# Kernel optimization log

Measured on AMD Instinct MI355X. Metric: run time of the kernel, lower is better.

## Reference

```python
import jax, jax.numpy as jnp
import numpy as np

D = 2048  # input_dimensions (== seq_len, required by the module's math)
H = 8192  # hidden_dimensions
B = 4
S = D


def setup_inputs() -> dict:
    key = jax.random.key(0)
    ks = jax.random.split(key, 13)
    scale_in = 1.0 / np.sqrt(D)
    scale_hid = 1.0 / np.sqrt(H)
    def lin(k, fan_in, fan_out, s):
        return jax.random.normal(k, (fan_in, fan_out), jnp.float32) * s
    inp = {"x": jax.random.normal(ks[0], (B, S, D), jnp.float32)}
    names = ["q", "k", "v"]
    for i, n in enumerate(names):
        inp[f"{n}_w1"] = lin(ks[1 + 4 * i], D, H, scale_in)
        inp[f"{n}_b1"] = jnp.zeros((H,), jnp.float32)
        inp[f"{n}_w2"] = lin(ks[2 + 4 * i], H, D, scale_hid)
        inp[f"{n}_b2"] = jnp.zeros((D,), jnp.float32)
    return inp


def _mlp(x, w1, b1, w2, b2):
    # Linear(D,H) -> ReLU -> Linear(H,D)
    h = jax.nn.relu(jnp.einsum("bsd,dh->bsh", x, w1) + b1)
    return jnp.einsum("bsh,hd->bsd", h, w2) + b2


def reference(x, q_w1, q_b1, q_w2, q_b2, k_w1, k_b1, k_w2, k_b2,
              v_w1, v_b1, v_w2, v_b2):
    Q = _mlp(x, q_w1, q_b1, q_w2, q_b2)
    K = _mlp(x, k_w1, k_b1, k_w2, k_b2)
    V = _mlp(x, v_w1, v_b1, v_w2, v_b2)
    # scores: Q @ K^T  -> [B, S, S]  (no 1/sqrt(d) scaling in original)
    scores = jnp.einsum("bsd,btd->bst", Q, K)
    # nn.Softmax(dim=1): over axis 1 (rows), NOT the usual last axis
    probs = jax.nn.softmax(scores, axis=1)
    # original computes V @ probs (requires S == D)
    out = jnp.einsum("bsd,bdt->bst", V, probs)
    return out
```

## Files before the change

### kernel.cpp

```cpp
#include <hip/hip_runtime.h>
#include <cstdint>
#include <cstddef>

typedef __attribute__((ext_vector_type(8))) short short8;
typedef __attribute__((ext_vector_type(4))) short short4v;
typedef __attribute__((ext_vector_type(4))) float f32x4;
typedef __attribute__((ext_vector_type(4))) int i32x4;

#define DEV __device__ __forceinline__

constexpr int DD = 2048;
constexpr int HHID = 8192;
constexpr int BB = 4;
constexpr int SS = 2048;
constexpr size_t NX = (size_t)BB * SS * DD;
constexpr size_t NW = (size_t)DD * HHID;
constexpr size_t NH = (size_t)BB * SS * HHID;

constexpr size_t OFF_XH = 0;
constexpr size_t OFF_XL = OFF_XH + NX * 2;
constexpr size_t OFF_WH = OFF_XL + NX * 2;
constexpr size_t OFF_WL = OFF_WH + NW * 2;
constexpr size_t OFF_HH = OFF_WL + NW * 2;
constexpr size_t OFF_HL = OFF_HH + NH * 2;
constexpr size_t OFF_QH = OFF_HL + NH * 2;
constexpr size_t OFF_QL = OFF_QH + NX * 2;
constexpr size_t OFF_KH = OFF_QL + NX * 2;
constexpr size_t OFF_KL = OFF_KH + NX * 2;
constexpr size_t OFF_V  = OFF_KL + NX * 2;
constexpr size_t OFF_XS  = OFF_V + NX * 2;
constexpr size_t OFF_WMQ = OFF_XS + 32768;
constexpr size_t OFF_WMK = OFF_WMQ + 32768;
constexpr size_t WS_TOTAL = OFF_WMK + 32768;
constexpr size_t OFF_ST = OFF_HH;
constexpr size_t OFF_PT = OFF_HL;
constexpr size_t OFF_XA1 = OFF_XL;
constexpr size_t OFF_XA2 = OFF_XL + NX;
constexpr size_t OFF_WA1 = OFF_WL;
constexpr size_t OFF_WA2 = OFF_WL + NW;

__device__ __align__(256) unsigned char g_ws[WS_TOTAL];

DEV unsigned char* wsbase(unsigned char* p) { return p ? p : (unsigned char*)g_ws; }
DEV short f2bf(float v) { __bf16 b = (__bf16)v; return __builtin_bit_cast(short, b); }
DEV float bf2f(short s) { return (float)__builtin_bit_cast(__bf16, s); }

DEV void gl16(const short* g, short* l) {
  __builtin_amdgcn_global_load_lds((const __attribute__((address_space(1))) void*)g,
                                   (__attribute__((address_space(3))) void*)l, 16, 0, 0);
}
DEV void gl16b(const signed char* g, signed char* l) {
  __builtin_amdgcn_global_load_lds((const __attribute__((address_space(1))) void*)g,
                                   (__attribute__((address_space(3))) void*)l, 16, 0, 0);
}

__global__ void cast_hi_k(const float* __restrict__ x, unsigned char* wsb,
                          size_t oh, size_t n4) {
  unsigned char* ws = wsbase(wsb);
  short4v* OH = (short4v*)(ws + oh);
  const f32x4* X = (const f32x4*)x;
  for (size_t i = (size_t)blockIdx.x * blockDim.x + threadIdx.x; i < n4;
       i += (size_t)gridDim.x * blockDim.x) {
    const f32x4 v = X[i];
    short4v hs;
#pragma unroll
    for (int e = 0; e < 4; ++e) hs[e] = f2bf(v[e]);
    OH[i] = hs;
  }
}

__launch_bounds__(256)
__global__ void quant_x_k(const float* __restrict__ x, unsigned char* wsb,
// ... 6 lines not shown
  const float* xr = x + (size_t)row * 2048;
  const int tid = threadIdx.x, lane = tid & 63;
  const f32x4 v0 = *(const f32x4*)&xr[tid * 8];
  const f32x4 v1 = *(const f32x4*)&xr[tid * 8 + 4];
  float m = 0.0f;
#pragma unroll
  for (int e = 0; e < 4; ++e) m = fmaxf(m, fmaxf(fabsf(v0[e]), fabsf(v1[e])));
#pragma unroll
  for (int o = 32; o; o >>= 1) m = fmaxf(m, __shfl_xor(m, o));
  __shared__ float rb[4];
  if (lane == 0) rb[tid >> 6] = m;
  __syncthreads();
  m = fmaxf(fmaxf(rb[0], rb[1]), fmaxf(rb[2], rb[3]));
  const float inv = (m > 1e-30f) ? 127.0f / m : 0.0f;
  if (tid == 0) XS[row] = m * (1.0f / 127.0f);
  unsigned int w1a = 0, w1b = 0, w2a = 0, w2b = 0;
#pragma unroll
  for (int e = 0; e < 8; ++e) {
    const float xv = (e < 4) ? v0[e] : v1[e - 4];
    const float q = xv * inv;
    const float a1f = rintf(q);
    int ia2 = (int)rintf((q - a1f) * 256.0f);
    ia2 = ia2 > 127 ? 127 : (ia2 < -127 ? -127 : ia2);
    const unsigned int b1 = (unsigned char)(signed char)(int)a1f;
    const unsigned int b2 = (unsigned char)(signed char)ia2;
    if (e < 4) { w1a |= b1 << (8 * e); w2a |= b2 << (8 * e); }
    else       { w1b |= b1 << (8 * (e - 4)); w2b |= b2 << (8 * (e - 4)); }
  }
  const size_t o = (size_t)row * 2048 + tid * 8;
  *(unsigned int*)&A1[o] = w1a; *(unsigned int*)&A1[o + 4] = w1b;
  *(unsigned int*)&A2[o] = w2a; *(unsigned int*)&A2[o + 4] = w2b;
}

__launch_bounds__(256)
__global__ void colmax_k(const float* __restrict__ w, unsigned char* wsb,
                         size_t omax, int R, int C) {
  unsigned char* ws = wsbase(wsb);
  unsigned int* MX = (unsigned int*)(ws + omax);
  const int col = blockIdx.x * 256 + threadIdx.x;
  const int r0 = blockIdx.y * 128;
  float m = 0.0f;
  for (int r = 0; r < 128; ++r) m = fmaxf(m, fabsf(w[(size_t)(r0 + r) * C + col]));
  atomicMax(&MX[col], __float_as_uint(m));
}

__global__ void transpose_quant_k(const float* __restrict__ src, unsigned char* wsb,
                                  size_t oa1, size_t oa2, size_t omax, int R, int C) {
  __shared__ float t[32][33];
  unsigned char* ws = wsbase(wsb);
  signed char* A1 = (signed char*)(ws + oa1);
  signed char* A2 = (signed char*)(ws + oa2);
  const unsigned int* MX = (const unsigned int*)(ws + omax);
  const int c0 = blockIdx.x << 5, r0 = blockIdx.y << 5;
  const int x = threadIdx.x, y = threadIdx.y;
#pragma unroll
  for (int i = 0; i < 4; ++i) {
    const int rr = y + (i << 3);
    t[rr][x] = src[(size_t)(r0 + rr) * C + c0 + x];
  }
  __syncthreads();
#pragma unroll
  for (int i = 0; i < 4; ++i) {
    const int oc = y + (i << 3);
    const float v = t[x][oc];
    const float mx = __uint_as_float(MX[c0 + oc]);
    const float inv = (mx > 1e-30f) ? 127.0f / mx : 0.0f;
    const float q = v * inv;
    const float a1f = rintf(q);
    int ia2 = (int)rintf((q - a1f) * 256.0f);
    ia2 = ia2 > 127 ? 127 : (ia2 < -127 ? -127 : ia2);
    const size_t o = (size_t)(c0 + oc) * R + r0 + x;
    A1[o] = (signed char)(int)a1f;
    A2[o] = (signed char)ia2;
  }
}

__global__ void transpose_cast_k(const float* __restrict__ src, unsigned char* wsb,
                                 size_t oh, size_t ol, int R, int C, int do_split) {
  __shared__ float t[32][33];
  unsigned char* ws = wsbase(wsb);
  short* OH = (short*)(ws + oh);
  short* OL = (short*)(ws + ol);
  const int c0 = blockIdx.x << 5, r0 = blockIdx.y << 5;
  const int x = threadIdx.x, y = threadIdx.y;
#pragma unroll
  for (int i = 0; i < 4; ++i) {
    const int rr = y + (i << 3);
    t[rr][x] = src[(size_t)(r0 + rr) * C + c0 + x];
  }
  __syncthreads();
#pragma unroll
  for (int i = 0; i < 4; ++i) {
    const int oc = y + (i << 3);
    const float v = t[x][oc];
    const size_t o = (size_t)(c0 + oc) * R + r0 + x;
    const short hb = f2bf(v);
    OH[o] = hb;
    if (do_split) OL[o] = f2bf(v - bf2f(hb));
  }
}

DEV i32x4 mfma_i8(i32x4 a, i32x4 b, i32x4 c) {
  return __builtin_amdgcn_mfma_i32_16x16x64_i8(a, b, c, 0, 0, 0);
}
DEV i32x4 rfi8(const signed char* base, int lstride, int L, int row, int fg) {
  return *(const i32x4*)&base[L * lstride + row * 64 + ((fg ^ ((row >> 1) & 3)) << 4)];
}

__launch_bounds__(512, 2)
__global__ void gemm_i8_k(unsigned char* wsb,
                          size_t xa1o, size_t xa2o, size_t wa1o, size_t wa2o,
                          size_t xso, size_t wmo, const float* __restrict__ bias,
                          size_t ohOff, size_t olOff, int M, int N, int K,
                          int gx, int gxy) {
  __shared__ alignas(16) signed char lds8[114688];

  unsigned char* ws = wsbase(wsb);
  const int tid = threadIdx.x;
  const int lane = tid & 63;
  const int wave = tid >> 6;
  const int wm = (wave >> 2) << 6;
  const int wn = (wave & 3) << 6;
  const int fr = lane & 15;
  const int fg = lane >> 4;

  const int nwg = gridDim.x;
  const int q8 = nwg >> 3;
  const int id = (blockIdx.x & 7) * q8 + (blockIdx.x >> 3);
  const int by = id / gx;
  const int bx = id - by * gx;
  const int brow = by << 7;
  const int bcol = bx << 8;

  const signed char* Xa1 = (const signed char*)(ws + xa1o);
  const signed char* Xa2 = (const signed char*)(ws + xa2o);
  const signed char* Wa1 = (const signed char*)(ws + wa1o);
  const signed char* Wa2 = (const signed char*)(ws + wa2o);
  const float* XS = (const float*)(ws + xso);
  const unsigned int* WM = (const unsigned int*)(ws + wmo);

  const int ar = tid >> 2, ac = tid & 3;
  const size_t aOff = (size_t)(brow + ar) * K + ((ac ^ ((ar >> 1) & 3)) << 4);
  size_t bOff[2];
#pragma unroll
  for (int h = 0; h < 2; ++h) {
    const int G = tid + h * 512;
    const int r = G >> 2, c = G & 3;
    bOff[h] = (size_t)(bcol + r) * K + ((c ^ ((r >> 1) & 3)) << 4);
  }

  auto stageA = [&](int slotBase, int tt) {
    const int ko = tt * 64;
    gl16b(Xa1 + aOff + ko, &lds8[slotBase + (tid << 4)]);
    gl16b(Xa2 + aOff + ko, &lds8[slotBase + 8192 + (tid << 4)]);
  };
  auto stageB = [&](int slotBase, int tt) {
    const int ko = tt * 64;
#pragma unroll
    for (int h = 0; h < 2; ++h) {
      gl16b(Wa1 + bOff[h] + ko, &lds8[slotBase + ((tid + h * 512) << 4)]);
      gl16b(Wa2 + bOff[h] + ko, &lds8[slotBase + 16384 + ((tid + h * 512) << 4)]);
    }
  };

  const int nt = K / 64;
  i32x4 I1[4][4] = {};
  i32x4 I2[4][4] = {};

  stageA(0, 0);
  stageB(49152, 0);
  if (nt > 1) { stageA(16384, 1); stageB(49152 + 32768, 1); }
  if (nt > 1) { asm volatile("s_waitcnt vmcnt(6)" ::: "memory"); }
// ... 23 lines not shown
#pragma unroll
    for (int i = 0; i < 2; ++i)
#pragma unroll
      for (int j = 0; j < 4; ++j) {
        I1[i][j] = mfma_i8(af[i][0], bf[j][0], I1[i][j]);
        I2[i][j] = mfma_i8(af[i][0], bf[j][1], I2[i][j]);
        I2[i][j] = mfma_i8(af[i][1], bf[j][0], I2[i][j]);
      }
    __builtin_amdgcn_s_setprio(0);
    __builtin_amdgcn_s_barrier();

    asm volatile("" ::: "memory");
    if (pf) stageB(sB2, t + 2);
#pragma unroll
    for (int i = 0; i < 2; ++i) {
      af[i][0] = rfi8(aS, 8192, 0, wm + (2 + i) * 16 + fr, fg);
      af[i][1] = rfi8(aS, 8192, 1, wm + (2 + i) * 16 + fr, fg);
    }
    __builtin_amdgcn_s_setprio(1);
#pragma unroll
    for (int i = 0; i < 2; ++i)
#pragma unroll
      for (int j = 0; j < 4; ++j) {
        I1[2 + i][j] = mfma_i8(af[i][0], bf[j][0], I1[2 + i][j]);
        I2[2 + i][j] = mfma_i8(af[i][0], bf[j][1], I2[2 + i][j]);
        I2[2 + i][j] = mfma_i8(af[i][1], bf[j][0], I2[2 + i][j]);
      }
    __builtin_amdgcn_s_setprio(0);
    if (pf) { asm volatile("s_waitcnt vmcnt(6)" ::: "memory"); }
    else    { asm volatile("s_waitcnt vmcnt(0)" ::: "memory"); }
    __builtin_amdgcn_s_barrier();
  }

  short* ldsS = (short*)lds8;
  short* Oh = (short*)(ws + ohOff);
  short* Ol = (short*)(ws + olOff);
  const int fq4 = fg << 2;
#pragma unroll
  for (int rd = 0; rd < 2; ++rd) {
    __builtin_amdgcn_s_barrier();
#pragma unroll
    for (int i = 0; i < 4; ++i) {
      const int rl = wm + i * 16 + fq4;
      const f32x4 xs4 = *(const f32x4*)&XS[brow + rl];
#pragma unroll
      for (int j = 0; j < 4; ++j) {
        const int cl = wn + j * 16 + fr;
        const float wsc = __uint_as_float(WM[bcol + cl]) * (1.0f / 127.0f);
        const float bv = bias[bcol + cl];
#pragma unroll
        for (int e = 0; e < 4; ++e) {
          float u = ((float)I1[i][j][e] + (float)I2[i][j][e] * (1.0f / 256.0f)) *
                        (xs4[e] * wsc) + bv;
          u = fmaxf(u, 0.0f);
          short v;
          if (rd == 0) {
            v = f2bf(u);
          } else {
            const short hb = f2bf(u);
            v = f2bf(u - bf2f(hb));
          }
          ldsS[(rl + e) * 264 + cl] = v;
        }
      }
    }
    __builtin_amdgcn_s_barrier();
    short* gout = (rd == 0) ? Oh : Ol;
#pragma unroll
    for (int gi = 0; gi < 8; ++gi) {
      const int g = gi * 512 + tid;
      const int row = g >> 5, cg = g & 31;
      const short8 v = *(const short8*)&ldsS[row * 264 + cg * 8];
      *(short8*)&gout[(size_t)(brow + row) * N + bcol + cg * 8] = v;
    }
  }
}

constexpr int CH = 8192;

template <int NAB>
DEV short8 read_frag(const short* base, int row, int s, int fg) {
  if constexpr (NAB == 1) {
    return *(const short8*)&base[row * 64 + ((((s << 2) | fg) ^ (row & 7)) << 3)];
  } else {
    return *(const short8*)&base[s * CH + row * 32 + ((fg ^ ((row >> 1) & 3)) << 3)];
  }
}

DEV f32x4 mfma16(short8 a, short8 b, f32x4 c) {
  return __builtin_amdgcn_mfma_f32_16x16x32_bf16(a, b, c, 0, 0, 0);
}

template <int NAB>
DEV void read_half(const short* aBase, int base_row, int fr, int fg, short8 (&av)[4][2]) {
#pragma unroll
  for (int i = 0; i < 4; ++i) {
    const int row = base_row + i * 16 + fr;
    av[i][0] = read_frag<NAB>(aBase, row, 0, fg);
    av[i][1] = read_frag<NAB>(aBase, row, 1, fg);
  }
}

template <int NAB, int H>
DEV void mfma_half(f32x4 (&acc)[8][4], const short8 (&av)[4][2], const short8 (&bfr)[4][2]) {
#pragma unroll
  for (int i = 0; i < 4; ++i)
#pragma unroll
    for (int j = 0; j < 4; ++j) {
      if constexpr (NAB == 1) {
        acc[H * 4 + i][j] = mfma16(av[i][0], bfr[j][0], acc[H * 4 + i][j]);
        acc[H * 4 + i][j] = mfma16(av[i][1], bfr[j][1], acc[H * 4 + i][j]);
      } else {
        acc[H * 4 + i][j] = mfma16(av[i][0], bfr[j][0], acc[H * 4 + i][j]);
        acc[H * 4 + i][j] = mfma16(av[i][0], bfr[j][1], acc[H * 4 + i][j]);
        acc[H * 4 + i][j] = mfma16(av[i][1], bfr[j][0], acc[H * 4 + i][j]);
      }
    }
}

template <int NAB, bool RELU, int STORE>
__launch_bounds__(512, 2)
__global__ void gemm8_k(unsigned char* wsb,
                        size_t aoff0, size_t aoff1, size_t boff0, size_t boff1,
                        const float* __restrict__ bias,
                        size_t ooff0, size_t ooff1, float* __restrict__ optr,
                        int M, int N, int K, int gx, int gxy) {
  constexpr int BK = (NAB == 2) ? 32 : 64;
  __shared__ alignas(16) short lds[10 * CH];

  unsigned char* ws = wsbase(wsb);
  const int tid = threadIdx.x;
  const int lane = tid & 63;
  const int wave = tid >> 6;
  const int wm = (wave >> 2) << 7;
  const int wn = (wave & 3) << 6;

  const int nwg = gridDim.x;
  const int q8 = nwg >> 3;
  const int id = (blockIdx.x & 7) * q8 + (blockIdx.x >> 3);
  const int bz = id / gxy;
  const int rem = id - bz * gxy;
  const int by = rem / gx;
  const int bx = rem - by * gx;
  const int brow = by << 8;
  const int bcol = bx << 8;

  const size_t batchA = (size_t)bz * M * K;
  const size_t batchB = (size_t)bz * N * K;
  const short* A0 = (const short*)(ws + aoff0) + batchA;
  const short* A1 = (const short*)(ws + aoff1) + batchA;
  const short* B0g = (const short*)(ws + boff0) + batchB;
  const short* B1g = (const short*)(ws + boff1) + batchB;

  size_t aSrc[2][2], bSrc[2][2];
#pragma unroll
  for (int h = 0; h < 2; ++h) {
    const int G = tid + h * 512;
    if constexpr (NAB == 1) {
      const int r = G >> 3, c = G & 7;
#pragma unroll
      for (int qq = 0; qq < 2; ++qq) {
        aSrc[qq][h] = (size_t)(brow + qq * 128 + r) * K + (size_t)((c ^ (r & 7)) << 3);
        bSrc[qq][h] = (size_t)(bcol + qq * 128 + r) * K + (size_t)((c ^ (r & 7)) << 3);
      }
    } else {
      const int r = G >> 2, c = G & 3;
      const size_t sw = (size_t)((c ^ ((r >> 1) & 3)) << 3);
      aSrc[0][h] = aSrc[1][h] = (size_t)(brow + r) * K + sw;
      bSrc[0][h] = bSrc[1][h] = (size_t)(bcol + r) * K + sw;
    }
  }
  const int ldst0 = tid << 3;

  auto issueA = [&](int slot, int qq, int tt) {
    short* dst = &lds[slot + qq * CH];
    const short* sp = (NAB == 2) ? (qq ? A1 : A0) : A0;
    const size_t ka = (size_t)tt * BK;
    gl16(sp + aSrc[qq][0] + ka, dst + ldst0);
    gl16(sp + aSrc[qq][1] + ka, dst + ldst0 + CH / 2);
  };
  auto issueB = [&](int slot, int qq, int tt) {
    short* dst = &lds[slot + qq * CH];
    const short* sp = (NAB == 2) ? (qq ? B1g : B0g) : B0g;
    const size_t ka = (size_t)tt * BK;
    gl16(sp + bSrc[qq][0] + ka, dst + ldst0);
    gl16(sp + bSrc[qq][1] + ka, dst + ldst0 + CH / 2);
  };

  const int nt = K / BK;
  const int fr = lane & 15;
  const int fg = lane >> 4;

  f32x4 acc[8][4] = {};

  issueA(0, 0, 0); issueA(0, 1, 0);
  issueB(6 * CH, 0, 0); issueB(6 * CH, 1, 0);
  if (nt > 1) {
    issueA(2 * CH, 0, 1); issueA(2 * CH, 1, 1);
    issueB(8 * CH, 0, 1); issueB(8 * CH, 1, 1);
    asm volatile("s_waitcnt vmcnt(8)" ::: "memory");
  } else {
    asm volatile("s_waitcnt vmcnt(0)" ::: "memory");
  }
  __builtin_amdgcn_s_barrier();

  for (int t = 0; t < nt; ++t) {
    const short* aBase = &lds[(t % 3) * (2 * CH)];
    const short* bBase = &lds[6 * CH + (t & 1) * (2 * CH)];
    const int sA2 = ((t + 2) % 3) * (2 * CH);
    const int sB  = 6 * CH + (t & 1) * (2 * CH);
    const bool pf = (t + 2 < nt);
    short8 bfr[4][2], av[4][2];

    if (pf) { issueA(sA2, 0, t + 2); issueA(sA2, 1, t + 2); }
#pragma unroll
    for (int j = 0; j < 4; ++j) {
      bfr[j][0] = read_frag<NAB>(bBase, wn + j * 16 + fr, 0, fg);
      bfr[j][1] = read_frag<NAB>(bBase, wn + j * 16 + fr, 1, fg);
    }
    read_half<NAB>(aBase, wm, fr, fg, av);
    __builtin_amdgcn_s_setprio(1);
    mfma_half<NAB, 0>(acc, av, bfr);
    __builtin_amdgcn_s_setprio(0);
    __builtin_amdgcn_s_barrier();

    asm volatile("" ::: "memory");
    if (pf) { issueB(sB, 0, t + 2); issueB(sB, 1, t + 2); }
    read_half<NAB>(aBase, wm + 64, fr, fg, av);
    __builtin_amdgcn_s_setprio(1);
    mfma_half<NAB, 1>(acc, av, bfr);
    __builtin_amdgcn_s_setprio(0);
    if (pf) {
      asm volatile("s_waitcnt vmcnt(8)" ::: "memory");
    } else {
      asm volatile("s_waitcnt vmcnt(0)" ::: "memory");
    }
    __builtin_amdgcn_s_barrier();
  }

  const int fq4 = (lane >> 4) << 2;
  if constexpr (STORE == 0 || STORE == 1) {
    short* Oh = (short*)(ws + ooff0);
    short* Ol = (short*)(ws + ooff1);
    constexpr int ROUNDS = (STORE == 0) ? 2 : 1;
#pragma unroll
    for (int rd = 0; rd < ROUNDS; ++rd) {
      __builtin_amdgcn_s_barrier();
#pragma unroll
      for (int i = 0; i < 8; ++i) {
        const int rl = wm + i * 16 + fq4;
#pragma unroll
        for (int j = 0; j < 4; ++j) {
          const int cl = wn + j * 16 + fr;
          const float bv = bias ? bias[bcol + cl] : 0.0f;
#pragma unroll
          for (int e = 0; e < 4; ++e) {
            float u = acc[i][j][e] + bv;
            if constexpr (RELU) u = fmaxf(u, 0.0f);
            short v;
            if (rd == 0) {
              v = f2bf(u);
            } else {
              const short hb = f2bf(u);
              v = f2bf(u - bf2f(hb));
            }
            lds[(rl + e) * 264 + cl] = v;
          }
        }
      }
      __builtin_amdgcn_s_barrier();
      short* gout = (rd == 0) ? Oh : Ol;
#pragma unroll
      for (int gi = 0; gi < 16; ++gi) {
        const int g = gi * 512 + tid;
        const int row = g >> 5, cg = g & 31;
        const short8 v = *(const short8*)&lds[row * 264 + cg * 8];
        *(short8*)&gout[(size_t)(brow + row) * N + bcol + cg * 8] = v;
      }
    }
  } else if constexpr (STORE == 2) {
    float* Of = (float*)(ws + ooff0) + (size_t)bz * M * N;
    float* ldsf = (float*)lds;
#pragma unroll
    for (int h = 0; h < 2; ++h) {
      __builtin_amdgcn_s_barrier();
      if ((wn & 128) == (h << 7)) {
#pragma unroll
        for (int i = 0; i < 8; ++i) {
          const int rl = wm + i * 16 + fq4;
#pragma unroll
          for (int j = 0; j < 4; ++j) {
            const int cp = (wn & 127) + j * 16 + fr;
#pragma unroll
            for (int e = 0; e < 4; ++e)
              ldsf[cp * 258 + rl + e] = acc[i][j][e];
          }
        }
      }
      __builtin_amdgcn_s_barrier();
#pragma unroll
      for (int gi = 0; gi < 16; ++gi) {
        const int g = gi * 512 + tid;
        const int tr = g >> 6, tc4 = (g & 63) << 2;
        const f32x4 v = *(const f32x4*)&ldsf[tr * 258 + tc4];
        *(f32x4*)&Of[(size_t)(bcol + h * 128 + tr) * M + brow + tc4] = v;
      }
    }
  } else {
    float* Op = optr + (size_t)bz * M * N;
    float* ldsf = (float*)lds;
#pragma unroll
    for (int h = 0; h < 2; ++h) {
      __builtin_amdgcn_s_barrier();
      if ((wm & 128) == (h << 7)) {
#pragma unroll
        for (int i = 0; i < 8; ++i) {
          const int rp = (wm & 127) + i * 16 + fq4;
#pragma unroll
          for (int j = 0; j < 4; ++j) {
            const int cl = wn + j * 16 + fr;
#pragma unroll
            for (int e = 0; e < 4; ++e)
              ldsf[(rp + e) * 258 + cl] = acc[i][j][e];
          }
        }
      }
      __builtin_amdgcn_s_barrier();
#pragma unroll
      for (int gi = 0; gi < 16; ++gi) {
        const int g = gi * 512 + tid;
        const int tr = g >> 6, tc4 = (g & 63) << 2;
        const f32x4 v = *(const f32x4*)&ldsf[tr * 258 + tc4];
        *(f32x4*)&Op[(size_t)(brow + h * 128 + tr) * N + bcol + tc4] = v;
      }
    }
  }
}

__launch_bounds__(256)
// ... 28 lines not shown
  short4v o1, o2;
#pragma unroll
  for (int q = 0; q < 4; ++q) { o1[q] = f2bf(e[q] * inv); o2[q] = f2bf(e[4 + q] * inv); }
  out[tid] = o1;
  out[tid + 256] = o2;
}

extern "C" void kernel_launch(void* const* d_in, const int* in_sizes, int n_in,
                              void* d_out, int out_size, void* d_ws, size_t ws_size,
                              hipStream_t stream) {
  const float* x   = (const float*)d_in[0];
  const float* qw1 = (const float*)d_in[1];
  const float* qb1 = (const float*)d_in[2];
  const float* qw2 = (const float*)d_in[3];
  const float* qb2 = (const float*)d_in[4];
  const float* kw1 = (const float*)d_in[5];
  const float* kb1 = (const float*)d_in[6];
  const float* kw2 = (const float*)d_in[7];
  const float* kb2 = (const float*)d_in[8];
  const float* vw1 = (const float*)d_in[9];
  const float* vb1 = (const float*)d_in[10];
  const float* vw2 = (const float*)d_in[11];
  const float* vb2 = (const float*)d_in[12];
  float* out = (float*)d_out;
  unsigned char* wsb = (ws_size >= WS_TOTAL) ? (unsigned char*)d_ws : nullptr;
  unsigned char* wsr;
  if (wsb) wsr = wsb;
  else { hipError_t e = hipGetSymbolAddress((void**)&wsr, HIP_SYMBOL(g_ws)); (void)e; }

  const int M = BB * SS;
  dim3 blk(512);
  dim3 tb(32, 8);

  hipMemsetAsync(wsr + OFF_WMQ, 0, 32768, stream);
  hipMemsetAsync(wsr + OFF_WMK, 0, 32768, stream);

  quant_x_k<<<8192, 256, 0, stream>>>(x, wsb, OFF_XA1, OFF_XA2, OFF_XS);
  cast_hi_k<<<4096, 256, 0, stream>>>(x, wsb, OFF_XH, NX / 4);

  colmax_k<<<dim3(HHID / 256, DD / 128), 256, 0, stream>>>(qw1, wsb, OFF_WMQ, DD, HHID);
  transpose_quant_k<<<dim3(HHID / 32, DD / 32), tb, 0, stream>>>(qw1, wsb, OFF_WA1, OFF_WA2, OFF_WMQ, DD, HHID);
  gemm_i8_k<<<2048, blk, 0, stream>>>(wsb, OFF_XA1, OFF_XA2, OFF_WA1, OFF_WA2,
                                      OFF_XS, OFF_WMQ, qb1, OFF_HH, OFF_HL,
                                      M, HHID, DD, 32, 2048);
  transpose_cast_k<<<dim3(DD / 32, HHID / 32), tb, 0, stream>>>(qw2, wsb, OFF_WH, OFF_WL, HHID, DD, 1);
  gemm8_k<2, false, 0><<<256, blk, 0, stream>>>(
      wsb, OFF_HH, OFF_HL, OFF_WH, OFF_WL, qb2, OFF_QH, OFF_QL, nullptr, M, DD, HHID, 8, 256);

  colmax_k<<<dim3(HHID / 256, DD / 128), 256, 0, stream>>>(kw1, wsb, OFF_WMK, DD, HHID);
  transpose_quant_k<<<dim3(HHID / 32, DD / 32), tb, 0, stream>>>(kw1, wsb, OFF_WA1, OFF_WA2, OFF_WMK, DD, HHID);
  gemm_i8_k<<<2048, blk, 0, stream>>>(wsb, OFF_XA1, OFF_XA2, OFF_WA1, OFF_WA2,
                                      OFF_XS, OFF_WMK, kb1, OFF_HH, OFF_HL,
                                      M, HHID, DD, 32, 2048);
  transpose_cast_k<<<dim3(DD / 32, HHID / 32), tb, 0, stream>>>(kw2, wsb, OFF_WH, OFF_WL, HHID, DD, 1);
  gemm8_k<2, false, 0><<<256, blk, 0, stream>>>(
      wsb, OFF_HH, OFF_HL, OFF_WH, OFF_WL, kb2, OFF_KH, OFF_KL, nullptr, M, DD, HHID, 8, 256);

  transpose_cast_k<<<dim3(HHID / 32, DD / 32), tb, 0, stream>>>(vw1, wsb, OFF_WH, OFF_WL, DD, HHID, 0);
  gemm8_k<1, true, 1><<<1024, blk, 0, stream>>>(
      wsb, OFF_XH, 0, OFF_WH, 0, vb1, OFF_HH, 0, nullptr, M, HHID, DD, 32, 1024);
  transpose_cast_k<<<dim3(DD / 32, HHID / 32), tb, 0, stream>>>(vw2, wsb, OFF_WH, OFF_WL, HHID, DD, 0);
  gemm8_k<1, false, 1><<<256, blk, 0, stream>>>(
      wsb, OFF_HH, 0, OFF_WH, 0, vb2, OFF_V, 0, nullptr, M, DD, HHID, 8, 256);

  gemm8_k<2, false, 2><<<256, blk, 0, stream>>>(
      wsb, OFF_QH, OFF_QL, OFF_KH, OFF_KL, nullptr, OFF_ST, 0, nullptr, SS, SS, DD, 8, 64);

  softmax_rows_k<<<BB * SS, 256, 0, stream>>>(wsb, OFF_ST, OFF_PT);

  gemm8_k<1, false, 3><<<256, blk, 0, stream>>>(
      wsb, OFF_V, 0, OFF_PT, 0, nullptr, 0, 0, out, SS, SS, DD, 8, 64);
}
```

Before: 3.066 ms.

## Move Q/K second-layer and score GEMMs from split-bf16 to split-int8 MFMA

Moves the Q and K second-layer GEMMs and the QK^T score GEMM off the three-pass split-bf16 path and onto the split-int8 (a1 + a2/256) MFMA kernel. To feed it, the change adds per-row quantization kernels for the hidden activations and for Q/K, per-column weight quantization for w2, a scale-fix pass, and a batched transposed fp32 store variant in gemm_i8_k. The aim is to replace three bf16 MFMAs per tile with two int8 MFMAs at higher throughput. In exchange it adds extra quantization passes over the large H buffer and changes numerical precision.

```diff
diff --git a/kernel.cpp b/kernel.cpp
--- a/kernel.cpp
+++ b/kernel.cpp
@@ -17,27 +17,31 @@
 constexpr size_t NW = (size_t)DD * HHID;
 constexpr size_t NH = (size_t)BB * SS * HHID;
 
-constexpr size_t OFF_XH = 0;
-constexpr size_t OFF_XL = OFF_XH + NX * 2;
-constexpr size_t OFF_WH = OFF_XL + NX * 2;
-constexpr size_t OFF_WL = OFF_WH + NW * 2;
-constexpr size_t OFF_HH = OFF_WL + NW * 2;
-constexpr size_t OFF_HL = OFF_HH + NH * 2;
-constexpr size_t OFF_QH = OFF_HL + NH * 2;
-constexpr size_t OFF_QL = OFF_QH + NX * 2;
-constexpr size_t OFF_KH = OFF_QL + NX * 2;
-constexpr size_t OFF_KL = OFF_KH + NX * 2;
-constexpr size_t OFF_V  = OFF_KL + NX * 2;
+constexpr size_t OFF_XH  = 0;
+constexpr size_t OFF_XA1 = OFF_XH + NX * 2;
+constexpr size_t OFF_XA2 = OFF_XA1 + NX;
+constexpr size_t OFF_WA1 = OFF_XA2 + NX;
+constexpr size_t OFF_WA2 = OFF_WA1 + NW;
+constexpr size_t OFF_WHV = OFF_WA1;
+constexpr size_t OFF_HH  = OFF_WA2 + NW;
+constexpr size_t OFF_HL  = OFF_HH + NH * 2;
+constexpr size_t OFF_QKH = OFF_HL + NH * 2;
+constexpr size_t OFF_QKL = OFF_QKH + NX * 2;
+constexpr size_t OFF_QA1 = OFF_QKL + NX * 2;
+constexpr size_t OFF_QA2 = OFF_QA1 + NX;
+constexpr size_t OFF_KA1 = OFF_QA2 + NX;
+constexpr size_t OFF_KA2 = OFF_KA1 + NX;
+constexpr size_t OFF_HA1 = OFF_KA2 + NX;
+constexpr size_t OFF_HA2 = OFF_HA1 + NH;
+constexpr size_t OFF_V   = OFF_HA2 + NH;
 constexpr size_t OFF_XS  = OFF_V + NX * 2;
-constexpr size_t OFF_WMQ = OFF_XS + 32768;
-constexpr size_t OFF_WMK = OFF_WMQ + 32768;
-constexpr size_t WS_TOTAL = OFF_WMK + 32768;
+constexpr size_t OFF_HS  = OFF_XS + 32768;
+constexpr size_t OFF_QS  = OFF_HS + 32768;
+constexpr size_t OFF_KS  = OFF_QS + 32768;
+constexpr size_t OFF_CM  = OFF_KS + 32768;
+constexpr size_t WS_TOTAL = OFF_CM + 32768;
 constexpr size_t OFF_ST = OFF_HH;
 constexpr size_t OFF_PT = OFF_HL;
-constexpr size_t OFF_XA1 = OFF_XL;
-constexpr size_t OFF_XA2 = OFF_XL + NX;
-constexpr size_t OFF_WA1 = OFF_WL;
-constexpr size_t OFF_WA2 = OFF_WL + NW;
 
 __device__ __align__(256) unsigned char g_ws[WS_TOTAL];
 
@@ -110,6 +114,48 @@
   *(unsigned int*)&A2[o] = w2a; *(unsigned int*)&A2[o + 4] = w2b;
 }
 
+__launch_bounds__(1024)
+__global__ void rowquant_k(unsigned char* wsb, size_t hho, size_t hlo,
+                           size_t oa1, size_t oa2, size_t oso, int rowlen) {
+  unsigned char* ws = wsbase(wsb);
+  const int row = blockIdx.x, tid = threadIdx.x, lane = tid & 63, wv = tid >> 6;
+  const int nw = blockDim.x >> 6;
+  const short8 hi = *((const short8*)((const short*)(ws + hho) + (size_t)row * rowlen) + tid);
+  const short8 lo = *((const short8*)((const short*)(ws + hlo) + (size_t)row * rowlen) + tid);
+  float v[8]; float m = 0.0f;
+#pragma unroll
+  for (int e = 0; e < 8; ++e) {
+    v[e] = bf2f(hi[e]) + bf2f(lo[e]);
+    m = fmaxf(m, fabsf(v[e]));
+  }
+#pragma unroll
+  for (int o = 32; o; o >>= 1) m = fmaxf(m, __shfl_xor(m, o));
+  __shared__ float rb[16];
+  if (lane == 0) rb[wv] = m;
+  __syncthreads();
+  m = rb[0];
+  for (int i = 1; i < nw; ++i) m = fmaxf(m, rb[i]);
+  const float inv = (m > 1e-30f) ? 127.0f / m : 0.0f;
+  if (tid == 0) ((float*)(ws + oso))[row] = m * (1.0f / 127.0f);
+  unsigned int w1a = 0, w1b = 0, w2a = 0, w2b = 0;
+#pragma unroll
+  for (int e = 0; e < 8; ++e) {
+    const float q = v[e] * inv;
+    const float a1f = rintf(q);
+    int ia2 = (int)rintf((q - a1f) * 256.0f);
+    ia2 = ia2 > 127 ? 127 : (ia2 < -127 ? -127 : ia2);
+    const unsigned int b1 = (unsigned char)(signed char)(int)a1f;
+    const unsigned int b2 = (unsigned char)(signed char)ia2;
+    if (e < 4) { w1a |= b1 << (8 * e); w2a |= b2 << (8 * e); }
+    else       { w1b |= b1 << (8 * (e - 4)); w2b |= b2 << (8 * (e - 4)); }
+  }
+  const size_t o = (size_t)row * rowlen + tid * 8;
+  signed char* A1 = (signed char*)(ws + oa1);
+  signed char* A2 = (signed char*)(ws + oa2);
+  *(unsigned int*)&A1[o] = w1a; *(unsigned int*)&A1[o + 4] = w1b;
+  *(unsigned int*)&A2[o] = w2a; *(unsigned int*)&A2[o + 4] = w2b;
+}
+
 __launch_bounds__(256)
 __global__ void colmax_k(const float* __restrict__ w, unsigned char* wsb,
                          size_t omax, int R, int C) {
@@ -122,13 +168,23 @@
   atomicMax(&MX[col], __float_as_uint(m));
 }
 
+__global__ void scalefix_k(unsigned char* wsb, size_t off, int n) {
+  unsigned char* ws = wsbase(wsb);
+  const int i = blockIdx.x * 256 + threadIdx.x;
+  if (i < n) {
+    float* p = (float*)(ws + off);
+    const unsigned int u = ((const unsigned int*)p)[i];
+    p[i] = __uint_as_float(u) * (1.0f / 127.0f);
+  }
+}
+
 __global__ void transpose_quant_k(const float* __restrict__ src, unsigned char* wsb,
-                                  size_t oa1, size_t oa2, size_t omax, int R, int C) {
+                                  size_t oa1, size_t oa2, size_t osc, int R, int C) {
   __shared__ float t[32][33];
   unsigned char* ws = wsbase(wsb);
   signed char* A1 = (signed char*)(ws + oa1);
   signed char* A2 = (signed char*)(ws + oa2);
-  const unsigned int* MX = (const unsigned int*)(ws + omax);
+  const float* SC = (const float*)(ws + osc);
   const int c0 = blockIdx.x << 5, r0 = blockIdx.y << 5;
   const int x = threadIdx.x, y = threadIdx.y;
 #pragma unroll
@@ -141,8 +197,8 @@
   for (int i = 0; i < 4; ++i) {
     const int oc = y + (i << 3);
     const float v = t[x][oc];
-    const float mx = __uint_as_float(MX[c0 + oc]);
-    const float inv = (mx > 1e-30f) ? 127.0f / mx : 0.0f;
+    const float s = SC[c0 + oc];
+    const float inv = (s > 1e-38f) ? 1.0f / s : 0.0f;
     const float q = v * inv;
     const float a1f = rintf(q);
     int ia2 = (int)rintf((q - a1f) * 256.0f);
@@ -154,11 +210,10 @@
 }
 
 __global__ void transpose_cast_k(const float* __restrict__ src, unsigned char* wsb,
-                                 size_t oh, size_t ol, int R, int C, int do_split) {
+                                 size_t oh, int R, int C) {
   __shared__ float t[32][33];
   unsigned char* ws = wsbase(wsb);
   short* OH = (short*)(ws + oh);
-  short* OL = (short*)(ws + ol);
   const int c0 = blockIdx.x << 5, r0 = blockIdx.y << 5;
   const int x = threadIdx.x, y = threadIdx.y;
 #pragma unroll
@@ -170,11 +225,7 @@
 #pragma unroll
   for (int i = 0; i < 4; ++i) {
     const int oc = y + (i << 3);
-    const float v = t[x][oc];
-    const size_t o = (size_t)(c0 + oc) * R + r0 + x;
-    const short hb = f2bf(v);
-    OH[o] = hb;
-    if (do_split) OL[o] = f2bf(v - bf2f(hb));
+    OH[(size_t)(c0 + oc) * R + r0 + x] = f2bf(t[x][oc]);
   }
 }
 
@@ -185,11 +236,12 @@
   return *(const i32x4*)&base[L * lstride + row * 64 + ((fg ^ ((row >> 1) & 3)) << 4)];
 }
 
+template <bool RELU, int STORE>
 __launch_bounds__(512, 2)
 __global__ void gemm_i8_k(unsigned char* wsb,
-                          size_t xa1o, size_t xa2o, size_t wa1o, size_t wa2o,
-                          size_t xso, size_t wmo, const float* __restrict__ bias,
-                          size_t ohOff, size_t olOff, int M, int N, int K,
+                          size_t a1o, size_t a2o, size_t b1o, size_t b2o,
+                          size_t aso, size_t bso, const float* __restrict__ bias,
+                          size_t o0, size_t o1, int M, int N, int K,
                           int gx, int gxy) {
   __shared__ alignas(16) signed char lds8[114688];
 
@@ -205,17 +257,21 @@
   const int nwg = gridDim.x;
   const int q8 = nwg >> 3;
   const int id = (blockIdx.x & 7) * q8 + (blockIdx.x >> 3);
-  const int by = id / gx;
-  const int bx = id - by * gx;
+  const int bz = id / gxy;
+  const int rem = id - bz * gxy;
+  const int by = rem / gx;
+  const int bx = rem - by * gx;
   const int brow = by << 7;
   const int bcol = bx << 8;
 
-  const signed char* Xa1 = (const signed char*)(ws + xa1o);
-  const signed char* Xa2 = (const signed char*)(ws + xa2o);
-  const signed char* Wa1 = (const signed char*)(ws + wa1o);
-  const signed char* Wa2 = (const signed char*)(ws + wa2o);
-  const float* XS = (const float*)(ws + xso);
-  const unsigned int* WM = (const unsigned int*)(ws + wmo);
+  const size_t batchA = (size_t)bz * M * K;
+  const size_t batchB = (STORE == 2) ? (size_t)bz * N * K : 0;
+  const signed char* Xa1 = (const signed char*)(ws + a1o) + batchA;
+  const signed char* Xa2 = (const signed char*)(ws + a2o) + batchA;
+  const signed char* Wa1 = (const signed char*)(ws + b1o) + batchB;
+  const signed char* Wa2 = (const signed char*)(ws + b2o) + batchB;
+  const float* AS = (const float*)(ws + aso) + (size_t)bz * M;
+  const float* BS = (const float*)(ws + bso) + ((STORE == 2) ? (size_t)bz * N : 0);
 
   const int ar = tid >> 2, ac = tid & 3;
   const size_t aOff = (size_t)(brow + ar) * K + ((ac ^ ((ar >> 1) & 3)) << 4);
@@ -305,100 +361,102 @@
     __builtin_amdgcn_s_barrier();
   }
 
-  short* ldsS = (short*)lds8;
-  short* Oh = (short*)(ws + ohOff);
-  short* Ol = (short*)(ws + olOff);
   const int fq4 = fg << 2;
-#pragma unroll
-  for (int rd = 0; rd < 2; ++rd) {
-    __builtin_amdgcn_s_barrier();
-#pragma unroll
-    for (int i = 0; i < 4; ++i) {
-      const int rl = wm + i * 16 + fq4;
-      const f32x4 xs4 = *(const f32x4*)&XS[brow + rl];
-#pragma unroll
-      for (int j = 0; j < 4; ++j) {
-        const int cl = wn + j * 16 + fr;
-        const float wsc = __uint_as_float(WM[bcol + cl]) * (1.0f / 127.0f);
-        const float bv = bias[bcol + cl];
-#pragma unroll
-        for (int e = 0; e < 4; ++e) {
-          float u = ((float)I1[i][j][e] + (float)I2[i][j][e] * (1.0f / 256.0f)) *
-                        (xs4[e] * wsc) + bv;
-          u = fmaxf(u, 0.0f);
-          short v;
-          if (rd == 0) {
-            v = f2bf(u);
-          } else {
-            const short hb = f2bf(u);
-            v = f2bf(u - bf2f(hb));
+  if constexpr (STORE == 0) {
+    short* ldsS = (short*)lds8;
+    short* Oh = (short*)(ws + o0);
+    short* Ol = (short*)(ws + o1);
+#pragma unroll
+    for (int rd = 0; rd < 2; ++rd) {
+      __builtin_amdgcn_s_barrier();
+#pragma unroll
+      for (int i = 0; i < 4; ++i) {
+        const int rl = wm + i * 16 + fq4;
+        const f32x4 sa4 = *(const f32x4*)&AS[brow + rl];
+#pragma unroll
+        for (int j = 0; j < 4; ++j) {
+          const int cl = wn + j * 16 + fr;
+          const float sb = BS[bcol + cl];
+          const float bv = bias ? bias[bcol + cl] : 0.0f;
+#pragma unroll
+          for (int e = 0; e < 4; ++e) {
+            float u = ((float)I1[i][j][e] + (float)I2[i][j][e] * (1.0f / 256.0f)) *
+                          (sa4[e] * sb) + bv;
+            if (RELU) u = fmaxf(u, 0.0f);
+            short v;
+            if (rd == 0) {
+              v = f2bf(u);
+            } else {
+              const short hb = f2bf(u);
+              v = f2bf(u - bf2f(hb));
+            }
+            ldsS[(rl + e) * 264 + cl] = v;
           }
-          ldsS[(rl + e) * 264 + cl] = v;
         }
       }
-    }
-    __builtin_amdgcn_s_barrier();
-    short* gout = (rd == 0) ? Oh : Ol;
-#pragma unroll
-    for (int gi = 0; gi < 8; ++gi) {
-      const int g = gi * 512 + tid;
-      const int row = g >> 5, cg = g & 31;
-      const short8 v = *(const short8*)&ldsS[row * 264 + cg * 8];
-      *(short8*)&gout[(size_t)(brow + row) * N + bcol + cg * 8] = v;
+      __builtin_amdgcn_s_barrier();
+      short* gout = (rd == 0) ? Oh : Ol;
+#pragma unroll
+      for (int gi = 0; gi < 8; ++gi) {
+        const int g = gi * 512 + tid;
+        const int row = g >> 5, cg = g & 31;
+        const short8 v = *(const short8*)&ldsS[row * 264 + cg * 8];
+        *(short8*)&gout[(size_t)(brow + row) * N + bcol + cg * 8] = v;
+      }
+    }
+  } else {
+    float* Of = (float*)(ws + o0) + (size_t)bz * M * N;
+    float* ldsf = (float*)lds8;
+#pragma unroll
+    for (int h2 = 0; h2 < 2; ++h2) {
+      __builtin_amdgcn_s_barrier();
+      if ((wn >> 7) == h2) {
+#pragma unroll
+        for (int i = 0; i < 4; ++i) {
+          const int rl = wm + i * 16 + fq4;
+          const f32x4 sa4 = *(const f32x4*)&AS[brow + rl];
+#pragma unroll
+          for (int j = 0; j < 4; ++j) {
+            const int cp = (wn & 127) + j * 16 + fr;
+            const float sb = BS[bcol + wn + j * 16 + fr];
+            f32x4 u;
+#pragma unroll
+            for (int e = 0; e < 4; ++e)
+              u[e] = ((float)I1[i][j][e] + (float)I2[i][j][e] * (1.0f / 256.0f)) *
+                     (sa4[e] * sb);
+            *(f32x4*)&ldsf[cp * 132 + rl] = u;
+          }
+        }
+      }
+      __builtin_amdgcn_s_barrier();
+#pragma unroll
+      for (int gi = 0; gi < 8; ++gi) {
+        const int g = gi * 512 + tid;
+        const int tr = g >> 5, tc4 = (g & 31) << 2;
+        const f32x4 v = *(const f32x4*)&ldsf[tr * 132 + tc4];
+        *(f32x4*)&Of[(size_t)(bcol + h2 * 128 + tr) * M + brow + tc4] = v;
+      }
     }
   }
 }
 
 constexpr int CH = 8192;
 
-template <int NAB>
-DEV short8 read_frag(const short* base, int row, int s, int fg) {
-  if constexpr (NAB == 1) {
-    return *(const short8*)&base[row * 64 + ((((s << 2) | fg) ^ (row & 7)) << 3)];
-  } else {
-    return *(const short8*)&base[s * CH + row * 32 + ((fg ^ ((row >> 1) & 3)) << 3)];
-  }
+DEV short8 read_frag1(const short* base, int row, int s, int fg) {
+  return *(const short8*)&base[row * 64 + ((((s << 2) | fg) ^ (row & 7)) << 3)];
 }
 
 DEV f32x4 mfma16(short8 a, short8 b, f32x4 c) {
   return __builtin_amdgcn_mfma_f32_16x16x32_bf16(a, b, c, 0, 0, 0);
 }
 
-template <int NAB>
-DEV void read_half(const short* aBase, int base_row, int fr, int fg, short8 (&av)[4][2]) {
-#pragma unroll
-  for (int i = 0; i < 4; ++i) {
-    const int row = base_row + i * 16 + fr;
-    av[i][0] = read_frag<NAB>(aBase, row, 0, fg);
-    av[i][1] = read_frag<NAB>(aBase, row, 1, fg);
-  }
-}
-
-template <int NAB, int H>
-DEV void mfma_half(f32x4 (&acc)[8][4], const short8 (&av)[4][2], const short8 (&bfr)[4][2]) {
-#pragma unroll
-  for (int i = 0; i < 4; ++i)
-#pragma unroll
-    for (int j = 0; j < 4; ++j) {
-      if constexpr (NAB == 1) {
-        acc[H * 4 + i][j] = mfma16(av[i][0], bfr[j][0], acc[H * 4 + i][j]);
-        acc[H * 4 + i][j] = mfma16(av[i][1], bfr[j][1], acc[H * 4 + i][j]);
-      } else {
-        acc[H * 4 + i][j] = mfma16(av[i][0], bfr[j][0], acc[H * 4 + i][j]);
-        acc[H * 4 + i][j] = mfma16(av[i][0], bfr[j][1], acc[H * 4 + i][j]);
-        acc[H * 4 + i][j] = mfma16(av[i][1], bfr[j][0], acc[H * 4 + i][j]);
-      }
-    }
-}
-
-template <int NAB, bool RELU, int STORE>
+template <bool RELU, int STORE>
 __launch_bounds__(512, 2)
 __global__ void gemm8_k(unsigned char* wsb,
-                        size_t aoff0, size_t aoff1, size_t boff0, size_t boff1,
+                        size_t aoff0, size_t boff0,
                         const float* __restrict__ bias,
-                        size_t ooff0, size_t ooff1, float* __restrict__ optr,
+                        size_t ooff0, float* __restrict__ optr,
                         int M, int N, int K, int gx, int gxy) {
-  constexpr int BK = (NAB == 2) ? 32 : 64;
   __shared__ alignas(16) short lds[10 * CH];
 
   unsigned char* ws = wsbase(wsb);
@@ -418,49 +476,36 @@
   const int brow = by << 8;
   const int bcol = bx << 8;
 
-  const size_t batchA = (size_t)bz * M * K;
-  const size_t batchB = (size_t)bz * N * K;
-  const short* A0 = (const short*)(ws + aoff0) + batchA;
-  const short* A1 = (const short*)(ws + aoff1) + batchA;
-  const short* B0g = (const short*)(ws + boff0) + batchB;
-  const short* B1g = (const short*)(ws + boff1) + batchB;
+  const short* A0 = (const short*)(ws + aoff0) + (size_t)bz * M * K;
+  const short* B0g = (const short*)(ws + boff0) + (size_t)bz * N * K;
 
   size_t aSrc[2][2], bSrc[2][2];
 #pragma unroll
   for (int h = 0; h < 2; ++h) {
     const int G = tid + h * 512;
-    if constexpr (NAB == 1) {
-      const int r = G >> 3, c = G & 7;
-#pragma unroll
-      for (int qq = 0; qq < 2; ++qq) {
-        aSrc[qq][h] = (size_t)(brow + qq * 128 + r) * K + (size_t)((c ^ (r & 7)) << 3);
-        bSrc[qq][h] = (size_t)(bcol + qq * 128 + r) * K + (size_t)((c ^ (r & 7)) << 3);
-      }
-    } else {
-      const int r = G >> 2, c = G & 3;
-      const size_t sw = (size_t)((c ^ ((r >> 1) & 3)) << 3);
-      aSrc[0][h] = aSrc[1][h] = (size_t)(brow + r) * K + sw;
-      bSrc[0][h] = bSrc[1][h] = (size_t)(bcol + r) * K + sw;
+    const int r = G >> 3, c = G & 7;
+#pragma unroll
+    for (int qq = 0; qq < 2; ++qq) {
+      aSrc[qq][h] = (size_t)(brow + qq * 128 + r) * K + (size_t)((c ^ (r & 7)) << 3);
+      bSrc[qq][h] = (size_t)(bcol + qq * 128 + r) * K + (size_t)((c ^ (r & 7)) << 3);
     }
   }
   const int ldst0 = tid << 3;
 
   auto issueA = [&](int slot, int qq, int tt) {
     short* dst = &lds[slot + qq * CH];
-    const short* sp = (NAB == 2) ? (qq ? A1 : A0) : A0;
-    const size_t ka = (size_t)tt * BK;
-    gl16(sp + aSrc[qq][0] + ka, dst + ldst0);
-    gl16(sp + aSrc[qq][1] + ka, dst + ldst0 + CH / 2);
+    const size_t ka = (size_t)tt * 64;
+    gl16(A0 + aSrc[qq][0] + ka, dst + ldst0);
+    gl16(A0 + aSrc[qq][1] + ka, dst + ldst0 + CH / 2);
   };
   auto issueB = [&](int slot, int qq, int tt) {
     short* dst = &lds[slot + qq * CH];
-    const short* sp = (NAB == 2) ? (qq ? B1g : B0g) : B0g;
-    const size_t ka = (size_t)tt * BK;
-    gl16(sp + bSrc[qq][0] + ka, dst + ldst0);
-    gl16(sp + bSrc[qq][1] + ka, dst + ldst0 + CH / 2);
+    const size_t ka = (size_t)tt * 64;
+    gl16(B0g + bSrc[qq][0] + ka, dst + ldst0);
+    gl16(B0g + bSrc[qq][1] + ka, dst + ldst0 + CH / 2);
   };
 
-  const int nt = K / BK;
+  const int nt = K / 64;
   const int fr = lane & 15;
   const int fg = lane >> 4;
 
@@ -488,20 +533,40 @@
     if (pf) { issueA(sA2, 0, t + 2); issueA(sA2, 1, t + 2); }
 #pragma unroll
     for (int j = 0; j < 4; ++j) {
-      bfr[j][0] = read_frag<NAB>(bBase, wn + j * 16 + fr, 0, fg);
-      bfr[j][1] = read_frag<NAB>(bBase, wn + j * 16 + fr, 1, fg);
-    }
-    read_half<NAB>(aBase, wm, fr, fg, av);
+      bfr[j][0] = read_frag1(bBase, wn + j * 16 + fr, 0, fg);
+      bfr[j][1] = read_frag1(bBase, wn + j * 16 + fr, 1, fg);
+    }
+#pragma unroll
+    for (int i = 0; i < 4; ++i) {
+      av[i][0] = read_frag1(aBase, wm + i * 16 + fr, 0, fg);
+      av[i][1] = read_frag1(aBase, wm + i * 16 + fr, 1, fg);
+    }
     __builtin_amdgcn_s_setprio(1);
-    mfma_half<NAB, 0>(acc, av, bfr);
+#pragma unroll
+    for (int i = 0; i < 4; ++i)
+#pragma unroll
+      for (int j = 0; j < 4; ++j) {
+        acc[i][j] = mfma16(av[i][0], bfr[j][0], acc[i][j]);
+        acc[i][j] = mfma16(av[i][1], bfr[j][1], acc[i][j]);
+      }
     __builtin_amdgcn_s_setprio(0);
     __builtin_amdgcn_s_barrier();
 
     asm volatile("" ::: "memory");
     if (pf) { issueB(sB, 0, t + 2); issueB(sB, 1, t + 2); }
-    read_half<NAB>(aBase, wm + 64, fr, fg, av);
+#pragma unroll
+    for (int i = 0; i < 4; ++i) {
+      av[i][0] = read_frag1(aBase, wm + 64 + i * 16 + fr, 0, fg);
+      av[i][1] = read_frag1(aBase, wm + 64 + i * 16 + fr, 1, fg);
+    }
     __builtin_amdgcn_s_setprio(1);
-    mfma_half<NAB, 1>(acc, av, bfr);
+#pragma unroll
+    for (int i = 0; i < 4; ++i)
+#pragma unroll
+      for (int j = 0; j < 4; ++j) {
+        acc[4 + i][j] = mfma16(av[i][0], bfr[j][0], acc[4 + i][j]);
+        acc[4 + i][j] = mfma16(av[i][1], bfr[j][1], acc[4 + i][j]);
+      }
     __builtin_amdgcn_s_setprio(0);
     if (pf) {
       asm volatile("s_waitcnt vmcnt(8)" ::: "memory");
@@ -512,72 +577,31 @@
   }
 
   const int fq4 = (lane >> 4) << 2;
-  if constexpr (STORE == 0 || STORE == 1) {
+  if constexpr (STORE == 1) {
     short* Oh = (short*)(ws + ooff0);
-    short* Ol = (short*)(ws + ooff1);
-    constexpr int ROUNDS = (STORE == 0) ? 2 : 1;
-#pragma unroll
-    for (int rd = 0; rd < ROUNDS; ++rd) {
-      __builtin_amdgcn_s_barrier();
-#pragma unroll
-      for (int i = 0; i < 8; ++i) {
-        const int rl = wm + i * 16 + fq4;
-#pragma unroll
-        for (int j = 0; j < 4; ++j) {
-          const int cl = wn + j * 16 + fr;
-          const float bv = bias ? bias[bcol + cl] : 0.0f;
-#pragma unroll
-          for (int e = 0; e < 4; ++e) {
-            float u = acc[i][j][e] + bv;
-            if constexpr (RELU) u = fmaxf(u, 0.0f);
-            short v;
-            if (rd == 0) {
-              v = f2bf(u);
-            } else {
-              const short hb = f2bf(u);
-              v = f2bf(u - bf2f(hb));
-            }
-            lds[(rl + e) * 264 + cl] = v;
-          }
+    __builtin_amdgcn_s_barrier();
+#pragma unroll
+    for (int i = 0; i < 8; ++i) {
+      const int rl = wm + i * 16 + fq4;
+#pragma unroll
+      for (int j = 0; j < 4; ++j) {
+        const int cl = wn + j * 16 + fr;
+        const float bv = bias ? bias[bcol + cl] : 0.0f;
+#pragma unroll
+        for (int e = 0; e < 4; ++e) {
+          float u = acc[i][j][e] + bv;
+          if (RELU) u = fmaxf(u, 0.0f);
+          lds[(rl + e) * 264 + cl] = f2bf(u);
         }
       }
-      __builtin_amdgcn_s_barrier();
-      short* gout = (rd == 0) ? Oh : Ol;
-#pragma unroll
-      for (int gi = 0; gi < 16; ++gi) {
-        const int g = gi * 512 + tid;
-        const int row = g >> 5, cg = g & 31;
-        const short8 v = *(const short8*)&lds[row * 264 + cg * 8];
-        *(short8*)&gout[(size_t)(brow + row) * N + bcol + cg * 8] = v;
-      }
-    }
-  } else if constexpr (STORE == 2) {
-    float* Of = (float*)(ws + ooff0) + (size_t)bz * M * N;
-    float* ldsf = (float*)lds;
-#pragma unroll
-    for (int h = 0; h < 2; ++h) {
-      __builtin_amdgcn_s_barrier();
-      if ((wn & 128) == (h << 7)) {
-#pragma unroll
-        for (int i = 0; i < 8; ++i) {
-          const int rl = wm + i * 16 + fq4;
-#pragma unroll
-          for (int j = 0; j < 4; ++j) {
-            const int cp = (wn & 127) + j * 16 + fr;
-#pragma unroll
-            for (int e = 0; e < 4; ++e)
-              ldsf[cp * 258 + rl + e] = acc[i][j][e];
-          }
-        }
-      }
-      __builtin_amdgcn_s_barrier();
-#pragma unroll
-      for (int gi = 0; gi < 16; ++gi) {
-        const int g = gi * 512 + tid;
-        const int tr = g >> 6, tc4 = (g & 63) << 2;
-        const f32x4 v = *(const f32x4*)&ldsf[tr * 258 + tc4];
-        *(f32x4*)&Of[(size_t)(bcol + h * 128 + tr) * M + brow + tc4] = v;
-      }
+    }
+    __builtin_amdgcn_s_barrier();
+#pragma unroll
+    for (int gi = 0; gi < 16; ++gi) {
+      const int g = gi * 512 + tid;
+      const int row = g >> 5, cg = g & 31;
+      const short8 v = *(const short8*)&lds[row * 264 + cg * 8];
+      *(short8*)&Oh[(size_t)(brow + row) * N + bcol + cg * 8] = v;
     }
   } else {
     float* Op = optr + (size_t)bz * M * N;
@@ -672,42 +696,56 @@
   dim3 blk(512);
   dim3 tb(32, 8);
 
-  hipMemsetAsync(wsr + OFF_WMQ, 0, 32768, stream);
-  hipMemsetAsync(wsr + OFF_WMK, 0, 32768, stream);
-
   quant_x_k<<<8192, 256, 0, stream>>>(x, wsb, OFF_XA1, OFF_XA2, OFF_XS);
   cast_hi_k<<<4096, 256, 0, stream>>>(x, wsb, OFF_XH, NX / 4);
 
-  colmax_k<<<dim3(HHID / 256, DD / 128), 256, 0, stream>>>(qw1, wsb, OFF_WMQ, DD, HHID);
-  transpose_quant_k<<<dim3(HHID / 32, DD / 32), tb, 0, stream>>>(qw1, wsb, OFF_WA1, OFF_WA2, OFF_WMQ, DD, HHID);
-  gemm_i8_k<<<2048, blk, 0, stream>>>(wsb, OFF_XA1, OFF_XA2, OFF_WA1, OFF_WA2,
-                                      OFF_XS, OFF_WMQ, qb1, OFF_HH, OFF_HL,
-                                      M, HHID, DD, 32, 2048);
-  transpose_cast_k<<<dim3(DD / 32, HHID / 32), tb, 0, stream>>>(qw2, wsb, OFF_WH, OFF_WL, HHID, DD, 1);
-  gemm8_k<2, false, 0><<<256, blk, 0, stream>>>(
-      wsb, OFF_HH, OFF_HL, OFF_WH, OFF_WL, qb2, OFF_QH, OFF_QL, nullptr, M, DD, HHID, 8, 256);
-
-  colmax_k<<<dim3(HHID / 256, DD / 128), 256, 0, stream>>>(kw1, wsb, OFF_WMK, DD, HHID);
-  transpose_quant_k<<<dim3(HHID / 32, DD / 32), tb, 0, stream>>>(kw1, wsb, OFF_WA1, OFF_WA2, OFF_WMK, DD, HHID);
-  gemm_i8_k<<<2048, blk, 0, stream>>>(wsb, OFF_XA1, OFF_XA2, OFF_WA1, OFF_WA2,
-                                      OFF_XS, OFF_WMK, kb1, OFF_HH, OFF_HL,
-                                      M, HHID, DD, 32, 2048);
-  transpose_cast_k<<<dim3(DD / 32, HHID / 32), tb, 0, stream>>>(kw2, wsb, OFF_WH, OFF_WL, HHID, DD, 1);
-  gemm8_k<2, false, 0><<<256, blk, 0, stream>>>(
-      wsb, OFF_HH, OFF_HL, OFF_WH, OFF_WL, kb2, OFF_KH, OFF_KL, nullptr, M, DD, HHID, 8, 256);
-
-  transpose_cast_k<<<dim3(HHID / 32, DD / 32), tb, 0, stream>>>(vw1, wsb, OFF_WH, OFF_WL, DD, HHID, 0);
-  gemm8_k<1, true, 1><<<1024, blk, 0, stream>>>(
-      wsb, OFF_XH, 0, OFF_WH, 0, vb1, OFF_HH, 0, nullptr, M, HHID, DD, 32, 1024);
-  transpose_cast_k<<<dim3(DD / 32, HHID / 32), tb, 0, stream>>>(vw2, wsb, OFF_WH, OFF_WL, HHID, DD, 0);
-  gemm8_k<1, false, 1><<<256, blk, 0, stream>>>(
-      wsb, OFF_HH, 0, OFF_WH, 0, vb2, OFF_V, 0, nullptr, M, DD, HHID, 8, 256);
-
-  gemm8_k<2, false, 2><<<256, blk, 0, stream>>>(
-      wsb, OFF_QH, OFF_QL, OFF_KH, OFF_KL, nullptr, OFF_ST, 0, nullptr, SS, SS, DD, 8, 64);
+  hipMemsetAsync(wsr + OFF_CM, 0, 32768, stream);
+  colmax_k<<<dim3(HHID / 256, DD / 128), 256, 0, stream>>>(qw1, wsb, OFF_CM, DD, HHID);
+  scalefix_k<<<32, 256, 0, stream>>>(wsb, OFF_CM, HHID);
+  transpose_quant_k<<<dim3(HHID / 32, DD / 32), tb, 0, stream>>>(qw1, wsb, OFF_WA1, OFF_WA2, OFF_CM, DD, HHID);
+  gemm_i8_k<true, 0><<<2048, blk, 0, stream>>>(wsb, OFF_XA1, OFF_XA2, OFF_WA1, OFF_WA2,
+                                               OFF_XS, OFF_CM, qb1, OFF_HH, OFF_HL,
+                                               M, HHID, DD, 32, 2048);
+  rowquant_k<<<8192, 1024, 0, stream>>>(wsb, OFF_HH, OFF_HL, OFF_HA1, OFF_HA2, OFF_HS, HHID);
+  hipMemsetAsync(wsr + OFF_CM, 0, 32768, stream);
+  colmax_k<<<dim3(DD / 256, HHID / 128), 256, 0, stream>>>(qw2, wsb, OFF_CM, HHID, DD);
+  scalefix_k<<<8, 256, 0, stream>>>(wsb, OFF_CM, DD);
+  transpose_quant_k<<<dim3(DD / 32, HHID / 32), tb, 0, stream>>>(qw2, wsb, OFF_WA1, OFF_WA2, OFF_CM, HHID, DD);
+  gemm_i8_k<false, 0><<<512, blk, 0, stream>>>(wsb, OFF_HA1, OFF_HA2, OFF_WA1, OFF_WA2,
+                                               OFF_HS, OFF_CM, qb2, OFF_QKH, OFF_QKL,
+                                               M, DD, HHID, 8, 512);
+  rowquant_k<<<8192, 256, 0, stream>>>(wsb, OFF_QKH, OFF_QKL, OFF_QA1, OFF_QA2, OFF_QS, DD);
+
+  hipMemsetAsync(wsr + OFF_CM, 0, 32768, stream);
+  colmax_k<<<dim3(HHID / 256, DD / 128), 256, 0, stream>>>(kw1, wsb, OFF_CM, DD, HHID);
+  scalefix_k<<<32, 256, 0, stream>>>(wsb, OFF_CM, HHID);
+  transpose_quant_k<<<dim3(HHID / 32, DD / 32), tb, 0, stream>>>(kw1, wsb, OFF_WA1, OFF_WA2, OFF_CM, DD, HHID);
+  gemm_i8_k<true, 0><<<2048, blk, 0, stream>>>(wsb, OFF_XA1, OFF_XA2, OFF_WA1, OFF_WA2,
+                                               OFF_XS, OFF_CM, kb1, OFF_HH, OFF_HL,
+                                               M, HHID, DD, 32, 2048);
+  rowquant_k<<<8192, 1024, 0, stream>>>(wsb, OFF_HH, OFF_HL, OFF_HA1, OFF_HA2, OFF_HS, HHID);
+  hipMemsetAsync(wsr + OFF_CM, 0, 32768, stream);
+  colmax_k<<<dim3(DD / 256, HHID / 128), 256, 0, stream>>>(kw2, wsb, OFF_CM, HHID, DD);
+  scalefix_k<<<8, 256, 0, stream>>>(wsb, OFF_CM, DD);
+  transpose_quant_k<<<dim3(DD / 32, HHID / 32), tb, 0, stream>>>(kw2, wsb, OFF_WA1, OFF_WA2, OFF_CM, HHID, DD);
+  gemm_i8_k<false, 0><<<512, blk, 0, stream>>>(wsb, OFF_HA1, OFF_HA2, OFF_WA1, OFF_WA2,
+                                               OFF_HS, OFF_CM, kb2, OFF_QKH, OFF_QKL,
+                                               M, DD, HHID, 8, 512);
+  rowquant_k<<<8192, 256, 0, stream>>>(wsb, OFF_QKH, OFF_QKL, OFF_KA1, OFF_KA2, OFF_KS, DD);
+
+  transpose_cast_k<<<dim3(HHID / 32, DD / 32), tb, 0, stream>>>(vw1, wsb, OFF_WHV, DD, HHID);
+  gemm8_k<true, 1><<<1024, blk, 0, stream>>>(
+      wsb, OFF_XH, OFF_WHV, vb1, OFF_HH, nullptr, M, HHID, DD, 32, 1024);
+  transpose_cast_k<<<dim3(DD / 32, HHID / 32), tb, 0, stream>>>(vw2, wsb, OFF_WHV, HHID, DD);
+  gemm8_k<false, 1><<<256, blk, 0, stream>>>(
+      wsb, OFF_HH, OFF_WHV, vb2, OFF_V, nullptr, M, DD, HHID, 8, 256);
+
+  gemm_i8_k<false, 2><<<512, blk, 0, stream>>>(wsb, OFF_QA1, OFF_QA2, OFF_KA1, OFF_KA2,
+                                               OFF_QS, OFF_KS, nullptr, OFF_ST, 0,
+                                               SS, SS, DD, 8, 128);
 
   softmax_rows_k<<<BB * SS, 256, 0, stream>>>(wsb, OFF_ST, OFF_PT);
 
-  gemm8_k<1, false, 3><<<256, blk, 0, stream>>>(
-      wsb, OFF_V, 0, OFF_PT, 0, nullptr, 0, 0, out, SS, SS, DD, 8, 64);
-}
+  gemm8_k<false, 3><<<256, blk, 0, stream>>>(
+      wsb, OFF_V, OFF_PT, nullptr, 0, out, SS, SS, DD, 8, 64);
+}
```

New measurement: 2.790 ms. -9.0%, faster.
